# Kernel optimization log

Measured on AMD Instinct MI355X. Metric: run time of the kernel, lower is better.

Reference implementation:

```python
import jax, jax.numpy as jnp
import numpy as np
from jax import lax

K = 20
ALPHA = 0.1
N_NODES = 100000
N_EDGES = 3200000


def setup_inputs() -> dict:
    key = jax.random.key(0)
    k1, k2, k3, k4, k5, k6 = jax.random.split(key, 6)
    x = jax.random.normal(k1, (N_NODES, 512), dtype=jnp.float32)
    edge_index = jax.random.randint(k2, (2, N_EDGES), 0, N_NODES, dtype=jnp.int32)
    W1 = jax.random.normal(k3, (512, 128), dtype=jnp.float32) * 0.05
    b1 = jax.random.normal(k4, (128,), dtype=jnp.float32) * 0.05
    W2 = jax.random.normal(k5, (128, 40), dtype=jnp.float32) * 0.05
    b2 = jax.random.normal(k6, (40,), dtype=jnp.float32) * 0.05
    return {"x": x, "edge_index": edge_index, "W1": W1, "b1": b1, "W2": W2, "b2": b2}


def reference(x, edge_index, W1, b1, W2, b2):
    N = x.shape[0]
    # MLP encoder (dropout is identity in eval mode)
    h = jax.nn.relu(x @ W1 + b1)          # [N, 128]
    h = jax.nn.relu(h @ W2 + b2)          # [N, num_classes]

    # gcn_norm with self-loops (PyG APPNP default: normalize=True, add_self_loops=True)
    loop = jnp.arange(N, dtype=edge_index.dtype)
    row = jnp.concatenate([edge_index[0], loop])  # source nodes
    col = jnp.concatenate([edge_index[1], loop])  # target nodes
    deg = jax.ops.segment_sum(jnp.ones_like(col, dtype=h.dtype), col, num_segments=N)
    dinv = jnp.where(deg > 0, lax.rsqrt(deg), 0.0)
    norm = dinv[row] * dinv[col]          # [E + N]

    h0 = h

    def step(z, _):
        msg = norm[:, None] * z[row]                       # gather + scale
        agg = jax.ops.segment_sum(msg, col, num_segments=N)  # scatter-add
        z = (1.0 - ALPHA) * agg + ALPHA * h0
        return z, None

    z, _ = lax.scan(step, h0, None, length=K)
    return z
```

## Files before the change

kernel.cpp:

```cpp
#include <hip/hip_runtime.h>
#include <hip/hip_bf16.h>

#define K_ITERS 20
#define F_IN 512
#define F_HID 128
#define F_OUT 40
#define SCAN_CHUNK 512


typedef const float __attribute__((address_space(1)))* glb_fp;
typedef float __attribute__((address_space(3)))* lds_fp;

__global__ void k_hist(const int* __restrict__ col, int E, int* __restrict__ cnt){
  int e = blockIdx.x*blockDim.x + threadIdx.x;
  if (e < E) atomicAdd(&cnt[col[e]], 1);
}

__global__ void k_dinv(const int* __restrict__ cnt, int N, float* __restrict__ dinv){
  int i = blockIdx.x*blockDim.x + threadIdx.x;
  if (i < N) dinv[i] = rsqrtf((float)(cnt[i] + 1));
}

__global__ void k_scan1(const int* __restrict__ cnt, int N, int* __restrict__ bsum){
  __shared__ int sd[256];
  int base = blockIdx.x * SCAN_CHUNK;
  int t = threadIdx.x;
  int i0 = base + 2*t, i1 = i0+1;
  int s = ((i0<N)?cnt[i0]:0) + ((i1<N)?cnt[i1]:0);
  sd[t] = s; __syncthreads();
  for (int off=1; off<256; off<<=1){
    int v = (t>=off)? sd[t-off] : 0;
    __syncthreads();
    sd[t] += v;
    __syncthreads();
  }
  if (t==255) bsum[blockIdx.x] = sd[255];
}
__global__ void k_scan2(const int* __restrict__ bsum, int NB, int* __restrict__ boff,
                        int* __restrict__ row_ptr, int N, int E){
  __shared__ int sd[256];
  int t = threadIdx.x;
  int v = (t < NB) ? bsum[t] : 0;
  sd[t] = v; __syncthreads();
  for (int off=1; off<256; off<<=1){
    int u = (t>=off)? sd[t-off] : 0;
    __syncthreads();
    sd[t] += u;
    __syncthreads();
  }
  if (t < NB) boff[t] = sd[t] - v;
  if (t == 0) row_ptr[N] = E;
}
__global__ void k_scan3(const int* __restrict__ cnt, int N, const int* __restrict__ boff,
                        int* __restrict__ row_ptr){
  __shared__ int sd[256];
  int base = blockIdx.x * SCAN_CHUNK;
  int t = threadIdx.x;
  int i0 = base + 2*t, i1 = i0+1;
  int c0 = (i0<N)?cnt[i0]:0, c1 = (i1<N)?cnt[i1]:0;
  int s = c0+c1;
  sd[t] = s; __syncthreads();
  for (int off=1; off<256; off<<=1){
    int v = (t>=off)? sd[t-off] : 0;
    __syncthreads();
    sd[t] += v;
    __syncthreads();
  }
  int excl = sd[t] - s + boff[blockIdx.x];
  if (i0<N) row_ptr[i0] = excl;
  if (i1<N) row_ptr[i1] = excl + c0;
}

__global__ void k_scatter(const int* __restrict__ row, const int* __restrict__ col, int E,
                          const int* __restrict__ row_ptr, int* __restrict__ cur,
                          const float* __restrict__ dinv,
                          int* __restrict__ csr_src, float* __restrict__ csr_norm){
  int e = blockIdx.x*blockDim.x + threadIdx.x;
  if (e >= E) return;
  int r = row[e], c = col[e];
  int p = row_ptr[c] + atomicAdd(&cur[c], 1);
  csr_src[p] = r;
  csr_norm[p] = dinv[r]*dinv[c];
}

__global__ __launch_bounds__(256) void k_mlp(const float* __restrict__ x,
                      const float* __restrict__ W1, const float* __restrict__ b1,
                      const float* __restrict__ W2, const float* __restrict__ b2,
                      float* __restrict__ h0, int N){
  __shared__ float lds[8704];
  const int t    = threadIdx.x;
  const int th   = t & 31;
  const int tn   = t >> 5;
  const int lane = t & 63;
  const int wv   = __builtin_amdgcn_readfirstlane(t >> 6);
  const int nb   = blockIdx.x * 64;

  const float* xp[8];
  #pragma unroll
  for (int j=0;j<8;++j){
    int r = nb + tn*8 + j; if (r >= N) r = N-1;
    const float* p = x + (size_t)r * F_IN;
    asm volatile("" : "+v"(p));
    xp[j] = p;
  }

  auto stage = [&](int kt, int b){
    const float* gs = W1 + kt*(32*128) + wv*1024 + lane*4;
    int lo = __builtin_amdgcn_readfirstlane((b*4096 + wv*1024) * 4);
    #pragma unroll
    for (int i=0;i<4;++i){
      __builtin_amdgcn_global_load_lds((glb_fp)(gs + i*256),
        (lds_fp)((char*)lds + lo + i*1024), 16, 0, 0);
    }
  };

  float acc[8][4];
  {
    float4 bb = *(const float4*)(b1 + th*4);
    #pragma unroll
    for (int j=0;j<8;++j){ acc[j][0]=bb.x; acc[j][1]=bb.y; acc[j][2]=bb.z; acc[j][3]=bb.w; }
  }

  stage(0, 0);
  __syncthreads();

  for (int kt=0; kt<16; ++kt){
    const int cur = kt & 1;
    if (kt < 15) stage(kt+1, cur^1);
    const int kbase = kt*32;
    #pragma unroll
    for (int c=0;c<8;++c){
      const int kb = kbase + c*4;
      float4 xv[8];
      #pragma unroll
      for (int j=0;j<8;++j) xv[j] = *(const float4*)(xp[j] + kb);
      const float* wl = lds + cur*4096 + c*512 + th*4;
      float4 wa = *(const float4*)(wl);
      float4 wb = *(const float4*)(wl + 128);
      float4 wc = *(const float4*)(wl + 256);
      float4 wd = *(const float4*)(wl + 384);
      #pragma unroll
      for (int j=0;j<8;++j){
        acc[j][0] += xv[j].x*wa.x; acc[j][1] += xv[j].x*wa.y; acc[j][2] += xv[j].x*wa.z; acc[j][3] += xv[j].x*wa.w;
        acc[j][0] += xv[j].y*wb.x; acc[j][1] += xv[j].y*wb.y; acc[j][2] += xv[j].y*wb.z; acc[j][3] += xv[j].y*wb.w;
        acc[j][0] += xv[j].z*wc.x; acc[j][1] += xv[j].z*wc.y; acc[j][2] += xv[j].z*wc.z; acc[j][3] += xv[j].z*wc.w;
        acc[j][0] += xv[j].w*wd.x; acc[j][1] += xv[j].w*wd.y; acc[j][2] += xv[j].w*wd.z; acc[j][3] += xv[j].w*wd.w;
      }
    }
    __syncthreads();
  }

  #pragma unroll
  for (int h=0; h<4; ++h){
    const int hid = th*4 + h;
    float4 v0 = make_float4(fmaxf(acc[0][h],0.f), fmaxf(acc[1][h],0.f),
                            fmaxf(acc[2][h],0.f), fmaxf(acc[3][h],0.f));
    float4 v1 = make_float4(fmaxf(acc[4][h],0.f), fmaxf(acc[5][h],0.f),
                            fmaxf(acc[6][h],0.f), fmaxf(acc[7][h],0.f));
    *(float4*)&lds[hid*68 + tn*8]     = v0;
    *(float4*)&lds[hid*68 + tn*8 + 4] = v1;
  }
  __syncthreads();

  const int c0 = wv*10;
  float a2[10];
  #pragma unroll
  for (int i=0;i<10;++i) a2[i] = b2[c0+i];
  #pragma unroll 4
  for (int k=0;k<F_HID;++k){
    const float hv = lds[k*68 + lane];
    #pragma unroll
    for (int i=0;i<10;++i) a2[i] += hv * W2[k*F_OUT + c0 + i];
  }
  const int gn = nb + lane;
  if (gn < N){
    float* o = h0 + (size_t)gn*F_OUT + c0;
    #pragma unroll
    for (int i=0;i<10;++i) o[i] = fmaxf(a2[i], 0.f);
  }
}

__global__ __launch_bounds__(256) void k_prop(const int* __restrict__ row_ptr, const int* __restrict__ csr_src,
                      const float* __restrict__ csr_norm, const float* __restrict__ dinv,
                      const float* __restrict__ zin, const float* __restrict__ h0,
                      float* __restrict__ zout, int N){
  const int wv   = __builtin_amdgcn_readfirstlane((int)(threadIdx.x >> 6));
  const int node = blockIdx.x*4 + wv;
  const int lane = threadIdx.x & 63;
  if (node >= N) return;
  if (lane >= F_OUT) return;
  const int beg = row_ptr[node], end = row_ptr[node+1];
  float acc = 0.f;
  int p = beg;

  int   cs[8]; float cn[8];
  bool have = (p + 8 <= end);
  if (have){
    #pragma unroll
    for (int j = 0; j < 8; j++){ cs[j] = csr_src[p+j]; cn[j] = csr_norm[p+j]; }
  }
  while (have){
    const int np = p + 8;
    const bool nh = (np + 8 <= end);
    int ns[8]; float nn[8];
    if (nh){
      #pragma unroll
      for (int j = 0; j < 8; j++){ ns[j] = csr_src[np+j]; nn[j] = csr_norm[np+j]; }
    }
    float z[8];
    #pragma unroll
    for (int j = 0; j < 8; j++) z[j] = zin[(size_t)cs[j]*F_OUT + lane];
    #pragma unroll
    for (int j = 0; j < 8; j++) acc += cn[j]*z[j];
    p = np; have = nh;
    if (nh){
      #pragma unroll
      for (int j = 0; j < 8; j++){ cs[j] = ns[j]; cn[j] = nn[j]; }
    }
  }
  for (; p < end; ++p)
    acc += csr_norm[p] * zin[(size_t)csr_src[p]*F_OUT + lane];

  const float di = dinv[node];
  const size_t idx = (size_t)node*F_OUT + lane;
  acc += di*di*zin[idx];
  zout[idx] = 0.9f*acc + 0.1f*h0[idx];
}

extern "C" void kernel_launch(void* const* d_in, const int* in_sizes, int n_in,
                              void* d_out, int out_size, void* d_ws, size_t ws_size,
                              hipStream_t stream){
  const float* x  = (const float*)d_in[0];
  const int*   ei = (const int*)d_in[1];
  const float* W1 = (const float*)d_in[2];
  const float* b1 = (const float*)d_in[3];
  const float* W2 = (const float*)d_in[4];
  const float* b2 = (const float*)d_in[5];
  int N = in_sizes[0] / F_IN;
  int E = in_sizes[1] / 2;
  const int* row = ei;
  const int* col = ei + E;

  char* w = (char*)d_ws;
  auto alloc = [&](size_t bytes)->void*{ void* p = w; w += (bytes + 255) & ~255ull; return p; };
  int*   cnt      = (int*)  alloc((size_t)N*4);
  int*   cur      = (int*)  alloc((size_t)N*4);
  int*   row_ptr  = (int*)  alloc(((size_t)N+1)*4);
  float* dinv     = (float*)alloc((size_t)N*4);
  int NB = (N + SCAN_CHUNK-1)/SCAN_CHUNK;
  int*   bsum     = (int*)  alloc((size_t)NB*4);
  int*   boff     = (int*)  alloc((size_t)NB*4);
  int*   csr_src  = (int*)  alloc((size_t)E*4);
  float* csr_norm = (float*)alloc((size_t)E*4);
  float* h0       = (float*)alloc((size_t)N*F_OUT*4);
  float* zA       = (float*)alloc((size_t)N*F_OUT*4);
  float* zB       = (float*)alloc((size_t)N*F_OUT*4);

  (void)hipMemsetAsync(cnt, 0, (size_t)N*4, stream);
  (void)hipMemsetAsync(cur, 0, (size_t)N*4, stream);

  int ge = (E + 255)/256;
  k_hist   <<<ge, 256, 0, stream>>>(col, E, cnt);
  k_dinv   <<<(N+255)/256, 256, 0, stream>>>(cnt, N, dinv);
  k_scan1  <<<NB, 256, 0, stream>>>(cnt, N, bsum);
  k_scan2  <<<1, 256, 0, stream>>>(bsum, NB, boff, row_ptr, N, E);
  k_scan3  <<<NB, 256, 0, stream>>>(cnt, N, boff, row_ptr);
  k_scatter<<<ge, 256, 0, stream>>>(row, col, E, row_ptr, cur, dinv, csr_src, csr_norm);

  k_mlp<<<(N+63)/64, 256, 0, stream>>>(x, W1, b1, W2, b2, h0, N);

  float* zi = h0; float* zo = zA;
  int gp = (N + 3)/4;
  for (int it=0; it<K_ITERS; ++it){
    float* dst = (it == K_ITERS-1) ? (float*)d_out : zo;
    k_prop<<<gp, 256, 0, stream>>>(row_ptr, csr_src, csr_norm, dinv, zi, h0, dst, N);
    float* nxt = (it==0) ? zB : zi;
    zi = zo; zo = nxt;
  }
}
```

Before: 2.851 ms.

## Pad CSR rows to multiples of eight, and read W1 directly in the MLP

Each node's CSR row is padded to a multiple of 8 edges, with zero norm and source 0 in the padding, which the memsets provide. This lets the propagation kernel run only full 8-edge chunks, double-buffering index loads and gathers with no scalar tail loop. The MLP kernel drops LDS staging of W1 through global_load_lds and instead reads W1 straight from global memory, with 16x8 per-thread tiles and double-buffered x loads. The tradeoffs are extra padded gathers (about 4 per node on average), two additional memsets, and more global or cache traffic for W1.

```diff
diff --git a/kernel.cpp b/kernel.cpp
--- a/kernel.cpp
+++ b/kernel.cpp
@@ -8,9 +8,6 @@
 #define SCAN_CHUNK 512
 
 
-typedef const float __attribute__((address_space(1)))* glb_fp;
-typedef float __attribute__((address_space(3)))* lds_fp;
-
 __global__ void k_hist(const int* __restrict__ col, int E, int* __restrict__ cnt){
   int e = blockIdx.x*blockDim.x + threadIdx.x;
   if (e < E) atomicAdd(&cnt[col[e]], 1);
@@ -26,7 +23,9 @@
   int base = blockIdx.x * SCAN_CHUNK;
   int t = threadIdx.x;
   int i0 = base + 2*t, i1 = i0+1;
-  int s = ((i0<N)?cnt[i0]:0) + ((i1<N)?cnt[i1]:0);
+  int c0 = (i0<N)? ((cnt[i0]+7)&~7) : 0;
+  int c1 = (i1<N)? ((cnt[i1]+7)&~7) : 0;
+  int s = c0 + c1;
   sd[t] = s; __syncthreads();
   for (int off=1; off<256; off<<=1){
     int v = (t>=off)? sd[t-off] : 0;
@@ -49,7 +48,7 @@
     __syncthreads();
   }
   if (t < NB) boff[t] = sd[t] - v;
-  if (t == 0) row_ptr[N] = E;
+  if (t == NB-1) row_ptr[N] = sd[t];
 }
 __global__ void k_scan3(const int* __restrict__ cnt, int N, const int* __restrict__ boff,
                         int* __restrict__ row_ptr){
@@ -57,7 +56,8 @@
   int base = blockIdx.x * SCAN_CHUNK;
   int t = threadIdx.x;
   int i0 = base + 2*t, i1 = i0+1;
-  int c0 = (i0<N)?cnt[i0]:0, c1 = (i1<N)?cnt[i1]:0;
+  int c0 = (i0<N)? ((cnt[i0]+7)&~7) : 0;
+  int c1 = (i1<N)? ((cnt[i1]+7)&~7) : 0;
   int s = c0+c1;
   sd[t] = s; __syncthreads();
   for (int off=1; off<256; off<<=1){
@@ -89,76 +89,73 @@
                       float* __restrict__ h0, int N){
   __shared__ float lds[8704];
   const int t    = threadIdx.x;
-  const int th   = t & 31;
-  const int tn   = t >> 5;
+  const int th   = t & 15;
+  const int tn   = t >> 4;
   const int lane = t & 63;
   const int wv   = __builtin_amdgcn_readfirstlane(t >> 6);
   const int nb   = blockIdx.x * 64;
 
-  const float* xp[8];
+  const float* xp[4];
   #pragma unroll
-  for (int j=0;j<8;++j){
-    int r = nb + tn*8 + j; if (r >= N) r = N-1;
+  for (int j=0;j<4;++j){
+    int r = nb + tn*4 + j; if (r >= N) r = N-1;
     const float* p = x + (size_t)r * F_IN;
     asm volatile("" : "+v"(p));
     xp[j] = p;
   }
 
-  auto stage = [&](int kt, int b){
-    const float* gs = W1 + kt*(32*128) + wv*1024 + lane*4;
-    int lo = __builtin_amdgcn_readfirstlane((b*4096 + wv*1024) * 4);
-    #pragma unroll
-    for (int i=0;i<4;++i){
-      __builtin_amdgcn_global_load_lds((glb_fp)(gs + i*256),
-        (lds_fp)((char*)lds + lo + i*1024), 16, 0, 0);
-    }
-  };
-
-  float acc[8][4];
+  float acc[4][8];
   {
-    float4 bb = *(const float4*)(b1 + th*4);
-    #pragma unroll
-    for (int j=0;j<8;++j){ acc[j][0]=bb.x; acc[j][1]=bb.y; acc[j][2]=bb.z; acc[j][3]=bb.w; }
-  }
-
-  stage(0, 0);
-  __syncthreads();
-
-  for (int kt=0; kt<16; ++kt){
-    const int cur = kt & 1;
-    if (kt < 15) stage(kt+1, cur^1);
-    const int kbase = kt*32;
-    #pragma unroll
-    for (int c=0;c<8;++c){
-      const int kb = kbase + c*4;
-      float4 xv[8];
+    const float4 ba = *(const float4*)(b1 + th*8);
+    const float4 bb = *(const float4*)(b1 + th*8 + 4);
+    #pragma unroll
+    for (int j=0;j<4;++j){
+      acc[j][0]=ba.x; acc[j][1]=ba.y; acc[j][2]=ba.z; acc[j][3]=ba.w;
+      acc[j][4]=bb.x; acc[j][5]=bb.y; acc[j][6]=bb.z; acc[j][7]=bb.w;
+    }
+  }
+
+  float4 xa[4], xb[4];
+  auto loadx = [&](float4 (&buf)[4], int gk){
+    const int kb = gk*4;
+    #pragma unroll
+    for (int j=0;j<4;++j) buf[j] = *(const float4*)(xp[j] + kb);
+  };
+  auto dochunk = [&](int gk, float4 (&xv)[4]){
+    const float* wl = W1 + gk*512 + th*8;
+    float w[4][8];
+    #pragma unroll
+    for (int r=0;r<4;++r){
+      *(float4*)&w[r][0] = *(const float4*)(wl + r*128);
+      *(float4*)&w[r][4] = *(const float4*)(wl + r*128 + 4);
+    }
+    float xk[4][4];
+    #pragma unroll
+    for (int j=0;j<4;++j){ float4 v = xv[j]; xk[j][0]=v.x; xk[j][1]=v.y; xk[j][2]=v.z; xk[j][3]=v.w; }
+    #pragma unroll
+    for (int r=0;r<4;++r){
       #pragma unroll
-      for (int j=0;j<8;++j) xv[j] = *(const float4*)(xp[j] + kb);
-      const float* wl = lds + cur*4096 + c*512 + th*4;
-      float4 wa = *(const float4*)(wl);
-      float4 wb = *(const float4*)(wl + 128);
-      float4 wc = *(const float4*)(wl + 256);
-      float4 wd = *(const float4*)(wl + 384);
-      #pragma unroll
-      for (int j=0;j<8;++j){
-        acc[j][0] += xv[j].x*wa.x; acc[j][1] += xv[j].x*wa.y; acc[j][2] += xv[j].x*wa.z; acc[j][3] += xv[j].x*wa.w;
-        acc[j][0] += xv[j].y*wb.x; acc[j][1] += xv[j].y*wb.y; acc[j][2] += xv[j].y*wb.z; acc[j][3] += xv[j].y*wb.w;
-        acc[j][0] += xv[j].z*wc.x; acc[j][1] += xv[j].z*wc.y; acc[j][2] += xv[j].z*wc.z; acc[j][3] += xv[j].z*wc.w;
-        acc[j][0] += xv[j].w*wd.x; acc[j][1] += xv[j].w*wd.y; acc[j][2] += xv[j].w*wd.z; acc[j][3] += xv[j].w*wd.w;
+      for (int j=0;j<4;++j){
+        #pragma unroll
+        for (int h=0;h<8;++h)
+          acc[j][h] += xk[j][r]*w[r][h];
       }
     }
-    __syncthreads();
+  };
+
+  loadx(xa, 0); loadx(xb, 1);
+  for (int gk=0; gk<128; gk+=2){
+    dochunk(gk, xa);
+    { int nk = gk+2; if (nk>127) nk = 127; loadx(xa, nk); }
+    dochunk(gk+1, xb);
+    { int nk = gk+3; if (nk>127) nk = 127; loadx(xb, nk); }
   }
 
   #pragma unroll
-  for (int h=0; h<4; ++h){
-    const int hid = th*4 + h;
-    float4 v0 = make_float4(fmaxf(acc[0][h],0.f), fmaxf(acc[1][h],0.f),
-                            fmaxf(acc[2][h],0.f), fmaxf(acc[3][h],0.f));
-    float4 v1 = make_float4(fmaxf(acc[4][h],0.f), fmaxf(acc[5][h],0.f),
-                            fmaxf(acc[6][h],0.f), fmaxf(acc[7][h],0.f));
-    *(float4*)&lds[hid*68 + tn*8]     = v0;
-    *(float4*)&lds[hid*68 + tn*8 + 4] = v1;
+  for (int h=0; h<8; ++h){
+    float4 v = make_float4(fmaxf(acc[0][h],0.f), fmaxf(acc[1][h],0.f),
+                           fmaxf(acc[2][h],0.f), fmaxf(acc[3][h],0.f));
+    *(float4*)&lds[(th*8+h)*68 + tn*4] = v;
   }
   __syncthreads();
 
@@ -189,42 +186,45 @@
   const int lane = threadIdx.x & 63;
   if (node >= N) return;
   if (lane >= F_OUT) return;
-  const int beg = row_ptr[node], end = row_ptr[node+1];
-  float acc = 0.f;
-  int p = beg;
-
-  int   cs[8]; float cn[8];
-  bool have = (p + 8 <= end);
-  if (have){
-    #pragma unroll
-    for (int j = 0; j < 8; j++){ cs[j] = csr_src[p+j]; cn[j] = csr_norm[p+j]; }
-  }
-  while (have){
-    const int np = p + 8;
-    const bool nh = (np + 8 <= end);
-    int ns[8]; float nn[8];
-    if (nh){
-      #pragma unroll
-      for (int j = 0; j < 8; j++){ ns[j] = csr_src[np+j]; nn[j] = csr_norm[np+j]; }
-    }
-    float z[8];
-    #pragma unroll
-    for (int j = 0; j < 8; j++) z[j] = zin[(size_t)cs[j]*F_OUT + lane];
-    #pragma unroll
-    for (int j = 0; j < 8; j++) acc += cn[j]*z[j];
-    p = np; have = nh;
-    if (nh){
-      #pragma unroll
-      for (int j = 0; j < 8; j++){ cs[j] = ns[j]; cn[j] = nn[j]; }
-    }
-  }
-  for (; p < end; ++p)
-    acc += csr_norm[p] * zin[(size_t)csr_src[p]*F_OUT + lane];
+  const int beg = row_ptr[node];
+  const int nch = (row_ptr[node+1] - beg) >> 3;
 
   const float di = dinv[node];
   const size_t idx = (size_t)node*F_OUT + lane;
-  acc += di*di*zin[idx];
-  zout[idx] = 0.9f*acc + 0.1f*h0[idx];
+  const float zself = zin[idx];
+  const float hh    = h0[idx];
+
+  auto loadm = [&](int (&S)[8], float (&Nm)[8], int P){
+    #pragma unroll
+    for (int j=0;j<8;j++){ S[j]=csr_src[P+j]; Nm[j]=csr_norm[P+j]; }
+  };
+  auto gath = [&](float (&Z)[8], const int (&S)[8]){
+    #pragma unroll
+    for (int j=0;j<8;j++){ Z[j]=zin[(size_t)S[j]*F_OUT + lane]; }
+  };
+
+  float acc = 0.f;
+  if (nch > 0){
+    int sA[8]; float nA[8]; float zvA[8];
+    int sB[8]; float nB[8]; float zvB[8];
+    loadm(sA, nA, beg); gath(zvA, sA);
+    int p = beg;
+    int c = 0;
+    while (true){
+      if (c+1 < nch){ loadm(sB, nB, p+8); gath(zvB, sB); }
+      #pragma unroll
+      for (int j=0;j<8;j++) acc += nA[j]*zvA[j];
+      if (++c >= nch) break;
+      if (c+1 < nch){ loadm(sA, nA, p+16); gath(zvA, sA); }
+      #pragma unroll
+      for (int j=0;j<8;j++) acc += nB[j]*zvB[j];
+      if (++c >= nch) break;
+      p += 16;
+    }
+  }
+
+  acc += di*di*zself;
+  zout[idx] = 0.9f*acc + 0.1f*hh;
 }
 
 extern "C" void kernel_launch(void* const* d_in, const int* in_sizes, int n_in,
@@ -240,6 +240,7 @@
   int E = in_sizes[1] / 2;
   const int* row = ei;
   const int* col = ei + E;
+  size_t EP = (size_t)E + 8*(size_t)N;
 
   char* w = (char*)d_ws;
   auto alloc = [&](size_t bytes)->void*{ void* p = w; w += (bytes + 255) & ~255ull; return p; };
@@ -250,14 +251,16 @@
   int NB = (N + SCAN_CHUNK-1)/SCAN_CHUNK;
   int*   bsum     = (int*)  alloc((size_t)NB*4);
   int*   boff     = (int*)  alloc((size_t)NB*4);
-  int*   csr_src  = (int*)  alloc((size_t)E*4);
-  float* csr_norm = (float*)alloc((size_t)E*4);
+  int*   csr_src  = (int*)  alloc(EP*4);
+  float* csr_norm = (float*)alloc(EP*4);
   float* h0       = (float*)alloc((size_t)N*F_OUT*4);
   float* zA       = (float*)alloc((size_t)N*F_OUT*4);
   float* zB       = (float*)alloc((size_t)N*F_OUT*4);
 
   (void)hipMemsetAsync(cnt, 0, (size_t)N*4, stream);
   (void)hipMemsetAsync(cur, 0, (size_t)N*4, stream);
+  (void)hipMemsetAsync(csr_src, 0, EP*4, stream);
+  (void)hipMemsetAsync(csr_norm, 0, EP*4, stream);
 
   int ge = (E + 255)/256;
   k_hist   <<<ge, 256, 0, stream>>>(col, E, cnt);
```

New measurement: 2.908 ms. 2.0% more time.

## Partition CSR by source block and sweep blocks in lockstep for gather locality

Applied to the files above, without the earlier changes.

Each destination's edge list is split into four segments by source-node range, each padded to a multiple of four with zeroed entries. The propagation kernel uses a fixed grid of 8192 waves, each owning up to 16 nodes, and walks all its nodes' segments one source block at a time. The goal is to keep concurrently gathered rows of z within about a quarter of the feature matrix so they stay in L2/MALL cache. The cost is a larger CSR with padding, extra memsets, 16 accumulators per thread that may limit occupancy, and less memory-level parallelism per node.

```diff
diff --git a/kernel.cpp b/kernel.cpp
--- a/kernel.cpp
+++ b/kernel.cpp
@@ -5,28 +5,41 @@
 #define F_IN 512
 #define F_HID 128
 #define F_OUT 40
-#define SCAN_CHUNK 512
+#define NBLK 4
+#define PWAVES 8192
+#define MAXK 16
 
 
 typedef const float __attribute__((address_space(1)))* glb_fp;
 typedef float __attribute__((address_space(3)))* lds_fp;
 
-__global__ void k_hist(const int* __restrict__ col, int E, int* __restrict__ cnt){
+__device__ __forceinline__ int blk_of(int s, int BS){
+  int b = (s >= 2*BS) ? 2 : 0;
+  if (s >= (b+1)*BS) b++;
+  return b;
+}
+
+__global__ void k_hist4(const int* __restrict__ row, const int* __restrict__ col,
+                        int E, int BS, int* __restrict__ cnt4){
   int e = blockIdx.x*blockDim.x + threadIdx.x;
-  if (e < E) atomicAdd(&cnt[col[e]], 1);
-}
-
-__global__ void k_dinv(const int* __restrict__ cnt, int N, float* __restrict__ dinv){
+  if (e < E) atomicAdd(&cnt4[col[e]*NBLK + blk_of(row[e], BS)], 1);
+}
+
+__global__ void k_dinv4(const int* __restrict__ cnt4, int N, float* __restrict__ dinv){
   int i = blockIdx.x*blockDim.x + threadIdx.x;
-  if (i < N) dinv[i] = rsqrtf((float)(cnt[i] + 1));
-}
-
-__global__ void k_scan1(const int* __restrict__ cnt, int N, int* __restrict__ bsum){
+  if (i < N){
+    int d = cnt4[i*NBLK] + cnt4[i*NBLK+1] + cnt4[i*NBLK+2] + cnt4[i*NBLK+3];
+    dinv[i] = rsqrtf((float)(d + 1));
+  }
+}
+
+__global__ void k_scan1(const int* __restrict__ cnt4, int M, int* __restrict__ bsum){
   __shared__ int sd[256];
-  int base = blockIdx.x * SCAN_CHUNK;
+  int base = blockIdx.x*2048 + threadIdx.x*8;
   int t = threadIdx.x;
-  int i0 = base + 2*t, i1 = i0+1;
-  int s = ((i0<N)?cnt[i0]:0) + ((i1<N)?cnt[i1]:0);
+  int s = 0;
+  #pragma unroll
+  for (int j=0;j<8;++j){ int i=base+j; if (i<M) s += (cnt4[i]+3)&~3; }
   sd[t] = s; __syncthreads();
   for (int off=1; off<256; off<<=1){
     int v = (t>=off)? sd[t-off] : 0;
@@ -37,7 +50,7 @@
   if (t==255) bsum[blockIdx.x] = sd[255];
 }
 __global__ void k_scan2(const int* __restrict__ bsum, int NB, int* __restrict__ boff,
-                        int* __restrict__ row_ptr, int N, int E){
+                        int* __restrict__ rp4, int M){
   __shared__ int sd[256];
   int t = threadIdx.x;
   int v = (t < NB) ? bsum[t] : 0;
@@ -49,16 +62,16 @@
     __syncthreads();
   }
   if (t < NB) boff[t] = sd[t] - v;
-  if (t == 0) row_ptr[N] = E;
-}
-__global__ void k_scan3(const int* __restrict__ cnt, int N, const int* __restrict__ boff,
-                        int* __restrict__ row_ptr){
+  if (t == NB-1) rp4[M] = sd[t];
+}
+__global__ void k_scan3(const int* __restrict__ cnt4, int M, const int* __restrict__ boff,
+                        int* __restrict__ rp4){
   __shared__ int sd[256];
-  int base = blockIdx.x * SCAN_CHUNK;
+  int base = blockIdx.x*2048 + threadIdx.x*8;
   int t = threadIdx.x;
-  int i0 = base + 2*t, i1 = i0+1;
-  int c0 = (i0<N)?cnt[i0]:0, c1 = (i1<N)?cnt[i1]:0;
-  int s = c0+c1;
+  int c[8]; int s = 0;
+  #pragma unroll
+  for (int j=0;j<8;++j){ int i=base+j; c[j] = (i<M)? ((cnt4[i]+3)&~3) : 0; s += c[j]; }
   sd[t] = s; __syncthreads();
   for (int off=1; off<256; off<<=1){
     int v = (t>=off)? sd[t-off] : 0;
@@ -66,19 +79,20 @@
     sd[t] += v;
     __syncthreads();
   }
-  int excl = sd[t] - s + boff[blockIdx.x];
-  if (i0<N) row_ptr[i0] = excl;
-  if (i1<N) row_ptr[i1] = excl + c0;
-}
-
-__global__ void k_scatter(const int* __restrict__ row, const int* __restrict__ col, int E,
-                          const int* __restrict__ row_ptr, int* __restrict__ cur,
-                          const float* __restrict__ dinv,
-                          int* __restrict__ csr_src, float* __restrict__ csr_norm){
+  int run = sd[t] - s + boff[blockIdx.x];
+  #pragma unroll
+  for (int j=0;j<8;++j){ int i=base+j; if (i<M) rp4[i] = run; run += c[j]; }
+}
+
+__global__ void k_scatter4(const int* __restrict__ row, const int* __restrict__ col, int E,
+                           int BS, const int* __restrict__ rp4, int* __restrict__ cur4,
+                           const float* __restrict__ dinv,
+                           int* __restrict__ csr_src, float* __restrict__ csr_norm){
   int e = blockIdx.x*blockDim.x + threadIdx.x;
   if (e >= E) return;
   int r = row[e], c = col[e];
-  int p = row_ptr[c] + atomicAdd(&cur[c], 1);
+  int seg = c*NBLK + blk_of(r, BS);
+  int p = rp4[seg] + atomicAdd(&cur4[seg], 1);
   csr_src[p] = r;
   csr_norm[p] = dinv[r]*dinv[c];
 }
@@ -180,51 +194,51 @@
   }
 }
 
-__global__ __launch_bounds__(256) void k_prop(const int* __restrict__ row_ptr, const int* __restrict__ csr_src,
-                      const float* __restrict__ csr_norm, const float* __restrict__ dinv,
-                      const float* __restrict__ zin, const float* __restrict__ h0,
-                      float* __restrict__ zout, int N){
+__global__ __launch_bounds__(256, 8) void k_prop(const int* __restrict__ rp4,
+                      const int* __restrict__ csr_src, const float* __restrict__ csr_norm,
+                      const float* __restrict__ dinv, const float* __restrict__ zin,
+                      const float* __restrict__ h0, float* __restrict__ zout,
+                      int N, int npw){
   const int wv   = __builtin_amdgcn_readfirstlane((int)(threadIdx.x >> 6));
-  const int node = blockIdx.x*4 + wv;
+  const int W    = blockIdx.x*4 + wv;
   const int lane = threadIdx.x & 63;
-  if (node >= N) return;
   if (lane >= F_OUT) return;
-  const int beg = row_ptr[node], end = row_ptr[node+1];
-  float acc = 0.f;
-  int p = beg;
-
-  int   cs[8]; float cn[8];
-  bool have = (p + 8 <= end);
-  if (have){
-    #pragma unroll
-    for (int j = 0; j < 8; j++){ cs[j] = csr_src[p+j]; cn[j] = csr_norm[p+j]; }
-  }
-  while (have){
-    const int np = p + 8;
-    const bool nh = (np + 8 <= end);
-    int ns[8]; float nn[8];
-    if (nh){
-      #pragma unroll
-      for (int j = 0; j < 8; j++){ ns[j] = csr_src[np+j]; nn[j] = csr_norm[np+j]; }
-    }
-    float z[8];
-    #pragma unroll
-    for (int j = 0; j < 8; j++) z[j] = zin[(size_t)cs[j]*F_OUT + lane];
-    #pragma unroll
-    for (int j = 0; j < 8; j++) acc += cn[j]*z[j];
-    p = np; have = nh;
-    if (nh){
-      #pragma unroll
-      for (int j = 0; j < 8; j++){ cs[j] = ns[j]; cn[j] = nn[j]; }
-    }
-  }
-  for (; p < end; ++p)
-    acc += csr_norm[p] * zin[(size_t)csr_src[p]*F_OUT + lane];
-
-  const float di = dinv[node];
-  const size_t idx = (size_t)node*F_OUT + lane;
-  acc += di*di*zin[idx];
-  zout[idx] = 0.9f*acc + 0.1f*h0[idx];
+
+  float acc[MAXK];
+  #pragma unroll
+  for (int k=0;k<MAXK;++k) acc[k] = 0.f;
+
+  for (int p=0; p<NBLK; ++p){
+    #pragma unroll
+    for (int k=0;k<MAXK;++k){
+      const int n = W + k*PWAVES;
+      if (k < npw && n < N){
+        const int beg = rp4[n*NBLK + p], end = rp4[n*NBLK + p + 1];
+        float a = 0.f;
+        for (int q=beg; q<end; q+=4){
+          int   s0=csr_src[q+0], s1=csr_src[q+1], s2=csr_src[q+2], s3=csr_src[q+3];
+          float m0=csr_norm[q+0], m1=csr_norm[q+1], m2=csr_norm[q+2], m3=csr_norm[q+3];
+          float z0 = zin[(size_t)s0*F_OUT + lane];
+          float z1 = zin[(size_t)s1*F_OUT + lane];
+          float z2 = zin[(size_t)s2*F_OUT + lane];
+          float z3 = zin[(size_t)s3*F_OUT + lane];
+          a += m0*z0; a += m1*z1; a += m2*z2; a += m3*z3;
+        }
+        acc[k] += a;
+      }
+    }
+  }
+
+  #pragma unroll
+  for (int k=0;k<MAXK;++k){
+    const int n = W + k*PWAVES;
+    if (k < npw && n < N){
+      const float di = dinv[n];
+      const size_t idx = (size_t)n*F_OUT + lane;
+      float v = acc[k] + di*di*zin[idx];
+      zout[idx] = 0.9f*v + 0.1f*h0[idx];
+    }
+  }
 }
 
 extern "C" void kernel_launch(void* const* d_in, const int* in_sizes, int n_in,
@@ -240,40 +254,45 @@
   int E = in_sizes[1] / 2;
   const int* row = ei;
   const int* col = ei + E;
+  const int BS = (N + NBLK - 1)/NBLK;
+  const int M  = N*NBLK;
+  size_t EP = (size_t)E + 3ull*M;
 
   char* w = (char*)d_ws;
   auto alloc = [&](size_t bytes)->void*{ void* p = w; w += (bytes + 255) & ~255ull; return p; };
-  int*   cnt      = (int*)  alloc((size_t)N*4);
-  int*   cur      = (int*)  alloc((size_t)N*4);
-  int*   row_ptr  = (int*)  alloc(((size_t)N+1)*4);
+  int*   cnt4     = (int*)  alloc((size_t)M*4);
+  int*   cur4     = (int*)  alloc((size_t)M*4);
+  int*   rp4      = (int*)  alloc(((size_t)M+1)*4);
   float* dinv     = (float*)alloc((size_t)N*4);
-  int NB = (N + SCAN_CHUNK-1)/SCAN_CHUNK;
+  int NB = (M + 2047)/2048;
   int*   bsum     = (int*)  alloc((size_t)NB*4);
   int*   boff     = (int*)  alloc((size_t)NB*4);
-  int*   csr_src  = (int*)  alloc((size_t)E*4);
-  float* csr_norm = (float*)alloc((size_t)E*4);
+  int*   csr_src  = (int*)  alloc(EP*4);
+  float* csr_norm = (float*)alloc(EP*4);
   float* h0       = (float*)alloc((size_t)N*F_OUT*4);
   float* zA       = (float*)alloc((size_t)N*F_OUT*4);
   float* zB       = (float*)alloc((size_t)N*F_OUT*4);
 
-  (void)hipMemsetAsync(cnt, 0, (size_t)N*4, stream);
-  (void)hipMemsetAsync(cur, 0, (size_t)N*4, stream);
+  (void)hipMemsetAsync(cnt4, 0, (size_t)M*4, stream);
+  (void)hipMemsetAsync(cur4, 0, (size_t)M*4, stream);
+  (void)hipMemsetAsync(csr_src, 0, EP*4, stream);
+  (void)hipMemsetAsync(csr_norm, 0, EP*4, stream);
 
   int ge = (E + 255)/256;
-  k_hist   <<<ge, 256, 0, stream>>>(col, E, cnt);
-  k_dinv   <<<(N+255)/256, 256, 0, stream>>>(cnt, N, dinv);
-  k_scan1  <<<NB, 256, 0, stream>>>(cnt, N, bsum);
-  k_scan2  <<<1, 256, 0, stream>>>(bsum, NB, boff, row_ptr, N, E);
-  k_scan3  <<<NB, 256, 0, stream>>>(cnt, N, boff, row_ptr);
-  k_scatter<<<ge, 256, 0, stream>>>(row, col, E, row_ptr, cur, dinv, csr_src, csr_norm);
+  k_hist4  <<<ge, 256, 0, stream>>>(row, col, E, BS, cnt4);
+  k_dinv4  <<<(N+255)/256, 256, 0, stream>>>(cnt4, N, dinv);
+  k_scan1  <<<NB, 256, 0, stream>>>(cnt4, M, bsum);
+  k_scan2  <<<1, 256, 0, stream>>>(bsum, NB, boff, rp4, M);
+  k_scan3  <<<NB, 256, 0, stream>>>(cnt4, M, boff, rp4);
+  k_scatter4<<<ge, 256, 0, stream>>>(row, col, E, BS, rp4, cur4, dinv, csr_src, csr_norm);
 
   k_mlp<<<(N+63)/64, 256, 0, stream>>>(x, W1, b1, W2, b2, h0, N);
 
+  int npw = (N + PWAVES - 1)/PWAVES;
   float* zi = h0; float* zo = zA;
-  int gp = (N + 3)/4;
   for (int it=0; it<K_ITERS; ++it){
     float* dst = (it == K_ITERS-1) ? (float*)d_out : zo;
-    k_prop<<<gp, 256, 0, stream>>>(row_ptr, csr_src, csr_norm, dinv, zi, h0, dst, N);
+    k_prop<<<PWAVES/4, 256, 0, stream>>>(rp4, csr_src, csr_norm, dinv, zi, h0, dst, N, npw);
     float* nxt = (it==0) ? zB : zi;
     zi = zo; zo = nxt;
   }
```

Result: faster. 2.763 ms (-3.1%).

## Pad CSR to six-edge groups and gather neighbor rows with float4 lanes

Applied to the files above, without the earlier changes.

Each node's CSR row is padded to a multiple of 6 entries, and source index and norm are interleaved into int2 pairs. The self-loop becomes a normal CSR entry, and padding is zero-filled so it contributes nothing. The propagation kernel now uses 60 lanes per wave: 6 edges at a time, each lane loading a float4 slice of a neighbor row, then an LDS reduction across the 6 edge groups, with a fixed pool of persistent waves. The MLP kernel also stages x tiles into LDS with async global-to-LDS loads instead of reading them directly from global memory. The aim is more memory-level parallelism and wider loads in the gather, at the cost of extra padded edges, a larger pair buffer and an extra memset.

```diff
diff --git a/kernel.cpp b/kernel.cpp
--- a/kernel.cpp
+++ b/kernel.cpp
@@ -5,7 +5,7 @@
 #define F_IN 512
 #define F_HID 128
 #define F_OUT 40
-#define SCAN_CHUNK 512
+#define PWAVES 8192
 
 
 typedef const float __attribute__((address_space(1)))* glb_fp;
@@ -21,12 +21,15 @@
   if (i < N) dinv[i] = rsqrtf((float)(cnt[i] + 1));
 }
 
+__device__ __forceinline__ int pad6(int c){ return ((c + 5)/6)*6; }
+
 __global__ void k_scan1(const int* __restrict__ cnt, int N, int* __restrict__ bsum){
   __shared__ int sd[256];
-  int base = blockIdx.x * SCAN_CHUNK;
+  int base = blockIdx.x*2048 + threadIdx.x*8;
   int t = threadIdx.x;
-  int i0 = base + 2*t, i1 = i0+1;
-  int s = ((i0<N)?cnt[i0]:0) + ((i1<N)?cnt[i1]:0);
+  int s = 0;
+  #pragma unroll
+  for (int j=0;j<8;++j){ int i=base+j; if (i<N) s += pad6(cnt[i]+1); }
   sd[t] = s; __syncthreads();
   for (int off=1; off<256; off<<=1){
     int v = (t>=off)? sd[t-off] : 0;
@@ -37,7 +40,7 @@
   if (t==255) bsum[blockIdx.x] = sd[255];
 }
 __global__ void k_scan2(const int* __restrict__ bsum, int NB, int* __restrict__ boff,
-                        int* __restrict__ row_ptr, int N, int E){
+                        int* __restrict__ rp, int N){
   __shared__ int sd[256];
   int t = threadIdx.x;
   int v = (t < NB) ? bsum[t] : 0;
@@ -49,16 +52,16 @@
     __syncthreads();
   }
   if (t < NB) boff[t] = sd[t] - v;
-  if (t == 0) row_ptr[N] = E;
+  if (t == NB-1) rp[N] = sd[t];
 }
 __global__ void k_scan3(const int* __restrict__ cnt, int N, const int* __restrict__ boff,
-                        int* __restrict__ row_ptr){
+                        int* __restrict__ rp){
   __shared__ int sd[256];
-  int base = blockIdx.x * SCAN_CHUNK;
+  int base = blockIdx.x*2048 + threadIdx.x*8;
   int t = threadIdx.x;
-  int i0 = base + 2*t, i1 = i0+1;
-  int c0 = (i0<N)?cnt[i0]:0, c1 = (i1<N)?cnt[i1]:0;
-  int s = c0+c1;
+  int c[8]; int s = 0;
+  #pragma unroll
+  for (int j=0;j<8;++j){ int i=base+j; c[j] = (i<N)? pad6(cnt[i]+1) : 0; s += c[j]; }
   sd[t] = s; __syncthreads();
   for (int off=1; off<256; off<<=1){
     int v = (t>=off)? sd[t-off] : 0;
@@ -66,28 +69,34 @@
     sd[t] += v;
     __syncthreads();
   }
-  int excl = sd[t] - s + boff[blockIdx.x];
-  if (i0<N) row_ptr[i0] = excl;
-  if (i1<N) row_ptr[i1] = excl + c0;
+  int run = sd[t] - s + boff[blockIdx.x];
+  #pragma unroll
+  for (int j=0;j<8;++j){ int i=base+j; if (i<N) rp[i] = run; run += c[j]; }
 }
 
 __global__ void k_scatter(const int* __restrict__ row, const int* __restrict__ col, int E,
-                          const int* __restrict__ row_ptr, int* __restrict__ cur,
-                          const float* __restrict__ dinv,
-                          int* __restrict__ csr_src, float* __restrict__ csr_norm){
+                          const int* __restrict__ rp, int* __restrict__ cur,
+                          const float* __restrict__ dinv, int2* __restrict__ pair){
   int e = blockIdx.x*blockDim.x + threadIdx.x;
   if (e >= E) return;
   int r = row[e], c = col[e];
-  int p = row_ptr[c] + atomicAdd(&cur[c], 1);
-  csr_src[p] = r;
-  csr_norm[p] = dinv[r]*dinv[c];
+  int p = rp[c] + atomicAdd(&cur[c], 1);
+  pair[p] = make_int2(r, __float_as_int(dinv[r]*dinv[c]));
+}
+__global__ void k_selfpair(int N, const int* __restrict__ rp, int* __restrict__ cur,
+                           const float* __restrict__ dinv, int2* __restrict__ pair){
+  int n = blockIdx.x*blockDim.x + threadIdx.x;
+  if (n >= N) return;
+  int p = rp[n] + atomicAdd(&cur[n], 1);
+  float di = dinv[n];
+  pair[p] = make_int2(n, __float_as_int(di*di));
 }
 
 __global__ __launch_bounds__(256) void k_mlp(const float* __restrict__ x,
                       const float* __restrict__ W1, const float* __restrict__ b1,
                       const float* __restrict__ W2, const float* __restrict__ b2,
                       float* __restrict__ h0, int N){
-  __shared__ float lds[8704];
+  __shared__ float lds[12288];
   const int t    = threadIdx.x;
   const int th   = t & 31;
   const int tn   = t >> 5;
@@ -95,16 +104,7 @@
   const int wv   = __builtin_amdgcn_readfirstlane(t >> 6);
   const int nb   = blockIdx.x * 64;
 
-  const float* xp[8];
-  #pragma unroll
-  for (int j=0;j<8;++j){
-    int r = nb + tn*8 + j; if (r >= N) r = N-1;
-    const float* p = x + (size_t)r * F_IN;
-    asm volatile("" : "+v"(p));
-    xp[j] = p;
-  }
-
-  auto stage = [&](int kt, int b){
+  auto stage_w = [&](int kt, int b){
     const float* gs = W1 + kt*(32*128) + wv*1024 + lane*4;
     int lo = __builtin_amdgcn_readfirstlane((b*4096 + wv*1024) * 4);
     #pragma unroll
@@ -113,6 +113,20 @@
         (lds_fp)((char*)lds + lo + i*1024), 16, 0, 0);
     }
   };
+  auto stage_x = [&](int kt, int b){
+    #pragma unroll
+    for (int s=0;s<2;++s){
+      int i = wv*2 + s;
+      int flat = i*256 + lane*4;
+      int n = flat >> 5;
+      int kk = flat & 31;
+      int node = nb + n; if (node >= N) node = N-1;
+      const float* gs = x + (size_t)node*F_IN + kt*32 + kk;
+      int lo = __builtin_amdgcn_readfirstlane(32768 + b*8192 + i*1024);
+      __builtin_amdgcn_global_load_lds((glb_fp)gs,
+        (lds_fp)((char*)lds + lo), 16, 0, 0);
+    }
+  };
 
   float acc[8][4];
   {
@@ -121,28 +135,28 @@
     for (int j=0;j<8;++j){ acc[j][0]=bb.x; acc[j][1]=bb.y; acc[j][2]=bb.z; acc[j][3]=bb.w; }
   }
 
-  stage(0, 0);
+  stage_w(0, 0); stage_x(0, 0);
   __syncthreads();
 
   for (int kt=0; kt<16; ++kt){
     const int cur = kt & 1;
-    if (kt < 15) stage(kt+1, cur^1);
-    const int kbase = kt*32;
+    if (kt < 15){ stage_w(kt+1, cur^1); stage_x(kt+1, cur^1); }
+    const float* xb = lds + 8192 + cur*2048;
+    const float* wb = lds + cur*4096;
     #pragma unroll
     for (int c=0;c<8;++c){
-      const int kb = kbase + c*4;
       float4 xv[8];
       #pragma unroll
-      for (int j=0;j<8;++j) xv[j] = *(const float4*)(xp[j] + kb);
-      const float* wl = lds + cur*4096 + c*512 + th*4;
+      for (int j=0;j<8;++j) xv[j] = *(const float4*)(xb + (tn*8+j)*32 + c*4);
+      const float* wl = wb + c*512 + th*4;
       float4 wa = *(const float4*)(wl);
-      float4 wb = *(const float4*)(wl + 128);
+      float4 wb4 = *(const float4*)(wl + 128);
       float4 wc = *(const float4*)(wl + 256);
       float4 wd = *(const float4*)(wl + 384);
       #pragma unroll
       for (int j=0;j<8;++j){
         acc[j][0] += xv[j].x*wa.x; acc[j][1] += xv[j].x*wa.y; acc[j][2] += xv[j].x*wa.z; acc[j][3] += xv[j].x*wa.w;
-        acc[j][0] += xv[j].y*wb.x; acc[j][1] += xv[j].y*wb.y; acc[j][2] += xv[j].y*wb.z; acc[j][3] += xv[j].y*wb.w;
+        acc[j][0] += xv[j].y*wb4.x; acc[j][1] += xv[j].y*wb4.y; acc[j][2] += xv[j].y*wb4.z; acc[j][3] += xv[j].y*wb4.w;
         acc[j][0] += xv[j].z*wc.x; acc[j][1] += xv[j].z*wc.y; acc[j][2] += xv[j].z*wc.z; acc[j][3] += xv[j].z*wc.w;
         acc[j][0] += xv[j].w*wd.x; acc[j][1] += xv[j].w*wd.y; acc[j][2] += xv[j].w*wd.z; acc[j][3] += xv[j].w*wd.w;
       }
@@ -180,51 +194,51 @@
   }
 }
 
-__global__ __launch_bounds__(256) void k_prop(const int* __restrict__ row_ptr, const int* __restrict__ csr_src,
-                      const float* __restrict__ csr_norm, const float* __restrict__ dinv,
-                      const float* __restrict__ zin, const float* __restrict__ h0,
-                      float* __restrict__ zout, int N){
+__global__ __launch_bounds__(256, 8) void k_prop(const int* __restrict__ rp,
+                      const int2* __restrict__ pair, const float* __restrict__ zin,
+                      const float* __restrict__ h0, float* __restrict__ zout,
+                      int N, int npw){
+  __shared__ float red[4][6][40];
   const int wv   = __builtin_amdgcn_readfirstlane((int)(threadIdx.x >> 6));
-  const int node = blockIdx.x*4 + wv;
+  const int W    = blockIdx.x*4 + wv;
   const int lane = threadIdx.x & 63;
-  if (node >= N) return;
-  if (lane >= F_OUT) return;
-  const int beg = row_ptr[node], end = row_ptr[node+1];
-  float acc = 0.f;
-  int p = beg;
-
-  int   cs[8]; float cn[8];
-  bool have = (p + 8 <= end);
-  if (have){
-    #pragma unroll
-    for (int j = 0; j < 8; j++){ cs[j] = csr_src[p+j]; cn[j] = csr_norm[p+j]; }
-  }
-  while (have){
-    const int np = p + 8;
-    const bool nh = (np + 8 <= end);
-    int ns[8]; float nn[8];
-    if (nh){
-      #pragma unroll
-      for (int j = 0; j < 8; j++){ ns[j] = csr_src[np+j]; nn[j] = csr_norm[np+j]; }
-    }
-    float z[8];
-    #pragma unroll
-    for (int j = 0; j < 8; j++) z[j] = zin[(size_t)cs[j]*F_OUT + lane];
-    #pragma unroll
-    for (int j = 0; j < 8; j++) acc += cn[j]*z[j];
-    p = np; have = nh;
-    if (nh){
-      #pragma unroll
-      for (int j = 0; j < 8; j++){ cs[j] = ns[j]; cn[j] = nn[j]; }
-    }
-  }
-  for (; p < end; ++p)
-    acc += csr_norm[p] * zin[(size_t)csr_src[p]*F_OUT + lane];
-
-  const float di = dinv[node];
-  const size_t idx = (size_t)node*F_OUT + lane;
-  acc += di*di*zin[idx];
-  zout[idx] = 0.9f*acc + 0.1f*h0[idx];
+  int e_lane = lane/10; if (e_lane > 5) e_lane = 5;
+  int qd = lane - e_lane*10; if (qd > 9) qd = 9;
+  const int qoff = qd*4;
+
+  for (int k=0; k<npw; ++k){
+    const int n = W + k*PWAVES;
+    if (n >= N) break;
+    const int beg = rp[n];
+    const int nch = (rp[n+1] - beg)/6;
+
+    float ax=0.f, ay=0.f, az=0.f, aw=0.f;
+    const int2* mp = pair + beg + e_lane;
+
+    int2 mA = mp[0];
+    float4 zA = *(const float4*)(zin + (size_t)mA.x*F_OUT + qoff);
+    int c = 0;
+    while (true){
+      int2 mB; float4 zB;
+      const bool hb = (c+1 < nch);
+      if (hb){
+        mB = mp[(c+1)*6];
+        zB = *(const float4*)(zin + (size_t)mB.x*F_OUT + qoff);
+      }
+      const float nm = __int_as_float(mA.y);
+      ax += nm*zA.x; ay += nm*zA.y; az += nm*zA.z; aw += nm*zA.w;
+      if (++c >= nch) break;
+      mA = mB; zA = zB;
+    }
+
+    if (lane < 60) *(float4*)&red[wv][e_lane][qoff] = make_float4(ax,ay,az,aw);
+    if (lane < F_OUT){
+      float s = red[wv][0][lane] + red[wv][1][lane] + red[wv][2][lane]
+              + red[wv][3][lane] + red[wv][4][lane] + red[wv][5][lane];
+      const size_t idx = (size_t)n*F_OUT + lane;
+      zout[idx] = 0.9f*s + 0.1f*h0[idx];
+    }
+  }
 }
 
 extern "C" void kernel_launch(void* const* d_in, const int* in_sizes, int n_in,
@@ -240,40 +254,42 @@
   int E = in_sizes[1] / 2;
   const int* row = ei;
   const int* col = ei + E;
+  size_t EP = (size_t)E + 7ull*(size_t)N;
 
   char* w = (char*)d_ws;
   auto alloc = [&](size_t bytes)->void*{ void* p = w; w += (bytes + 255) & ~255ull; return p; };
   int*   cnt      = (int*)  alloc((size_t)N*4);
   int*   cur      = (int*)  alloc((size_t)N*4);
-  int*   row_ptr  = (int*)  alloc(((size_t)N+1)*4);
+  int*   rp       = (int*)  alloc(((size_t)N+1)*4);
   float* dinv     = (float*)alloc((size_t)N*4);
-  int NB = (N + SCAN_CHUNK-1)/SCAN_CHUNK;
+  int NB = (N + 2047)/2048;
   int*   bsum     = (int*)  alloc((size_t)NB*4);
   int*   boff     = (int*)  alloc((size_t)NB*4);
-  int*   csr_src  = (int*)  alloc((size_t)E*4);
-  float* csr_norm = (float*)alloc((size_t)E*4);
+  int2*  pair     = (int2*) alloc(EP*8);
   float* h0       = (float*)alloc((size_t)N*F_OUT*4);
   float* zA       = (float*)alloc((size_t)N*F_OUT*4);
   float* zB       = (float*)alloc((size_t)N*F_OUT*4);
 
   (void)hipMemsetAsync(cnt, 0, (size_t)N*4, stream);
   (void)hipMemsetAsync(cur, 0, (size_t)N*4, stream);
+  (void)hipMemsetAsync(pair, 0, EP*8, stream);
 
   int ge = (E + 255)/256;
-  k_hist   <<<ge, 256, 0, stream>>>(col, E, cnt);
-  k_dinv   <<<(N+255)/256, 256, 0, stream>>>(cnt, N, dinv);
-  k_scan1  <<<NB, 256, 0, stream>>>(cnt, N, bsum);
-  k_scan2  <<<1, 256, 0, stream>>>(bsum, NB, boff, row_ptr, N, E);
-  k_scan3  <<<NB, 256, 0, stream>>>(cnt, N, boff, row_ptr);
-  k_scatter<<<ge, 256, 0, stream>>>(row, col, E, row_ptr, cur, dinv, csr_src, csr_norm);
+  k_hist    <<<ge, 256, 0, stream>>>(col, E, cnt);
+  k_dinv    <<<(N+255)/256, 256, 0, stream>>>(cnt, N, dinv);
+  k_scan1   <<<NB, 256, 0, stream>>>(cnt, N, bsum);
+  k_scan2   <<<1, 256, 0, stream>>>(bsum, NB, boff, rp, N);
+  k_scan3   <<<NB, 256, 0, stream>>>(cnt, N, boff, rp);
+  k_scatter <<<ge, 256, 0, stream>>>(row, col, E, rp, cur, dinv, pair);
+  k_selfpair<<<(N+255)/256, 256, 0, stream>>>(N, rp, cur, dinv, pair);
 
   k_mlp<<<(N+63)/64, 256, 0, stream>>>(x, W1, b1, W2, b2, h0, N);
 
+  int npw = (N + PWAVES - 1)/PWAVES;
   float* zi = h0; float* zo = zA;
-  int gp = (N + 3)/4;
   for (int it=0; it<K_ITERS; ++it){
     float* dst = (it == K_ITERS-1) ? (float*)d_out : zo;
-    k_prop<<<gp, 256, 0, stream>>>(row_ptr, csr_src, csr_norm, dinv, zi, h0, dst, N);
+    k_prop<<<PWAVES/4, 256, 0, stream>>>(rp, pair, zi, h0, dst, N, npw);
     float* nxt = (it==0) ? zB : zi;
     zi = zo; zo = nxt;
   }
```

After: 2.790 ms. -2.1%, faster.
